# Kernel tuning notes

Hardware: AMD Instinct MI355X
Metric: run time of the kernel (lower is better)

Reference implementation:

```python
import jax, jax.numpy as jnp
import numpy as np
from jax.ops import segment_sum

N_NODES = 300000
N_EDGES = 600000
N_GRAPHS = 12000
HIDDEN = 128
F_ATOM, V_ATOM, D_ATOM = 9, 119, 9
F_BOND, V_BOND, D_BOND = 3, 6, 3


def setup_inputs() -> dict:
    key = jax.random.key(0)
    ks = jax.random.split(key, 12)
    x = jax.random.randint(ks[0], (N_NODES, F_ATOM), 0, 100, dtype=jnp.int64 if jax.config.jax_enable_x64 else jnp.int32)
    edge_index = jax.random.randint(ks[1], (2, N_EDGES), 0, N_NODES)
    edge_attr = jax.random.randint(ks[2], (N_EDGES, F_BOND), 0, 5)
    batch = jnp.sort(jax.random.randint(ks[3], (N_NODES,), 0, N_GRAPHS))
    s = 0.02
    atom_emb = jax.random.normal(ks[4], (F_ATOM, V_ATOM, D_ATOM), jnp.float32) * s
    bond_emb = jax.random.normal(ks[5], (F_BOND, V_BOND, D_BOND), jnp.float32) * s
    W1 = jax.random.normal(ks[6], (D_ATOM, HIDDEN), jnp.float32) * (1.0 / np.sqrt(D_ATOM))
    b1 = jnp.zeros((HIDDEN,), jnp.float32)
    W2 = jax.random.normal(ks[7], (HIDDEN, HIDDEN), jnp.float32) * (1.0 / np.sqrt(HIDDEN))
    b2 = jnp.zeros((HIDDEN,), jnp.float32)
    Wfc = jax.random.normal(ks[8], (HIDDEN, 128), jnp.float32) * (1.0 / np.sqrt(HIDDEN))
    bfc = jnp.zeros((128,), jnp.float32)
    return {"x": x, "edge_index": edge_index, "edge_attr": edge_attr, "batch": batch,
            "atom_emb": atom_emb, "bond_emb": bond_emb,
            "W1": W1, "b1": b1, "W2": W2, "b2": b2, "Wfc": Wfc, "bfc": bfc}


def _multi_embed(tables, idx):
    # tables: [F, V, D], idx: [N, F] -> sum over F of tables[f, idx[:, f]] -> [N, D]
    F = tables.shape[0]
    gathered = tables[jnp.arange(F)[None, :], idx]  # [N, F, D]
    return gathered.sum(axis=1)


def _gcn_conv(h, edge_index, W, b, n_nodes):
    # PyG GCNConv: add self-loops, symmetric deg^-1/2 normalization
    src, dst = edge_index[0], edge_index[1]
    deg = segment_sum(jnp.ones(src.shape[0], h.dtype), dst, num_segments=n_nodes) + 1.0  # self-loop
    dinv = jax.lax.rsqrt(deg)
    h = h @ W  # transform before propagation
    coef = (dinv[src] * dinv[dst])[:, None]
    agg = segment_sum(h[src] * coef, dst, num_segments=n_nodes)
    agg = agg + h * (dinv * dinv)[:, None]  # self-loop contribution (norm = 1/deg)
    return agg + b


def reference(x, edge_index, edge_attr, batch, atom_emb, bond_emb, W1, b1, W2, b2, Wfc, bfc):
    h = _multi_embed(atom_emb, x)            # AtomEncoder: [N, 9]
    _ = _multi_embed(bond_emb, edge_attr)    # BondEncoder (computed, unused downstream)
    h = _gcn_conv(h, edge_index, W1, b1, N_NODES)
    h = jax.nn.relu(h)
    h = _gcn_conv(h, edge_index, W2, b2, N_NODES)
    # global_mean_pool over graphs
    sums = segment_sum(h, batch, num_segments=N_GRAPHS)
    cnt = segment_sum(jnp.ones(N_NODES, h.dtype), batch, num_segments=N_GRAPHS)
    graph_emb = sums / jnp.clip(cnt, 1.0)[:, None]
    return graph_emb @ Wfc + bfc
```

## Files before the change

### kernel.cpp

```cpp
#include <hip/hip_runtime.h>

#define NN 300000
#define NE 600000
#define NG 12000
#define HH 128
#define FA 9
#define VA 119
#define DA 9
#define NCHUNK ((NN + 1023) / 1024)
#define POISON 0xAAAAAAAAu

#define HB  64
#define NCB 1172

#define OEMB 0
#define OW1  (FA*VA*DA)
#define OB1  (OW1 + DA*HH)
#define OW2  (OB1 + HH)
#define OB2  (OW2 + HH*HH)
#define OWFC (OB2 + HH)
#define OBFC (OWFC + HH*HH)
#define NWC  (OBFC + HH)

typedef unsigned short u16;
typedef unsigned int u32;
typedef __attribute__((ext_vector_type(8))) short bfrag8;
typedef __attribute__((ext_vector_type(16))) float ffrag16;

__device__ __forceinline__ float bf2f(u16 u){
  union { u32 i; float f; } v; v.i = ((u32)u) << 16; return v.f;
}
__device__ __forceinline__ float bflo(u32 w){
  union { u32 i; float f; } v; v.i = w << 16; return v.f;
}
__device__ __forceinline__ float bfhi(u32 w){
  union { u32 i; float f; } v; v.i = w & 0xFFFF0000u; return v.f;
}
__device__ __forceinline__ u16 f2bf(float f){
  union { float f; u32 i; } v; v.f = f;
  u32 x = v.i;
  return (u16)((x + 0x7FFFu + ((x >> 16) & 1u)) >> 16);
}
__device__ __forceinline__ float ldf(const void* p, int i, int isf32){
  return isf32 ? ((const float*)p)[i] : bf2f(((const u16*)p)[i]);
}
__device__ __forceinline__ int detect_isf32(const u16* emb16, int t, int* scnt){
  if (t == 0) *scnt = 0;
  __syncthreads();
  u16 u = emb16[t];
  int e = (u >> 7) & 0xFF;
  if (e >= 96 && e < 126) atomicAdd(scnt, 1);
  __syncthreads();
  return (*scnt >= 200) ? 0 : 1;
}

__global__ void k_pre(const int* __restrict__ x, const void* emb, const void* W1,
                      const void* b1, const void* W2, const void* b2,
                      const void* Wfc, const void* bfc,
                      const int* __restrict__ batch, const int* __restrict__ dst,
                      int* __restrict__ flag, float* __restrict__ wc,
                      u32* __restrict__ degcur, u16* __restrict__ rank,
                      int* __restrict__ gstart, uint4* __restrict__ h0a,
                      u32* __restrict__ h0b, float* __restrict__ wcomb,
                      float* __restrict__ bcomb, u32* __restrict__ btab2){
  __shared__ float embS[FA * VA * DA];
  __shared__ int scnt;
  int t = threadIdx.x;

  if (blockIdx.x < HB){
    int htid = blockIdx.x * 256 + t;
    const int4* d4 = (const int4*)dst;
    uint2* r2 = (uint2*)rank;
    #pragma unroll 2
    for (int i = htid; i < NE / 4; i += HB * 256){
      int4 v = d4[i];
      u32 r0 = atomicAdd(&degcur[v.x], 1u);
      u32 r1 = atomicAdd(&degcur[v.y], 1u);
      u32 rr2 = atomicAdd(&degcur[v.z], 1u);
      u32 rr3 = atomicAdd(&degcur[v.w], 1u);
      uint2 pk;
      pk.x = (u32)(u16)(r0 - POISON) | (((u32)(u16)(r1 - POISON)) << 16);
      pk.y = (u32)(u16)(rr2 - POISON) | (((u32)(u16)(rr3 - POISON)) << 16);
      r2[i] = pk;
    }
    return;
  }

  int isf32 = detect_isf32((const u16*)emb, t, &scnt);
  int tid = (blockIdx.x - HB) * 256 + t;
  int nth = NCB * 256;
  if (tid == 0) flag[0] = isf32;

  if (isf32){
    const float4* e4 = (const float4*)emb;
    for (int i = t; i < (FA*VA*DA)/4; i += 256){
      float4 v = e4[i];
      int o = i * 4;
      embS[o+0] = v.x; embS[o+1] = v.y; embS[o+2] = v.z; embS[o+3] = v.w;
    }
    if (t < 3) embS[9636 + t] = ((const float*)emb)[9636 + t];
  } else {
    const uint4* e4 = (const uint4*)emb;
    for (int i = t; i < (FA*VA*DA)/8; i += 256){
      uint4 v = e4[i];
      int o = i * 8;
      embS[o+0] = bflo(v.x); embS[o+1] = bfhi(v.x);
      embS[o+2] = bflo(v.y); embS[o+3] = bfhi(v.y);
      embS[o+4] = bflo(v.z); embS[o+5] = bfhi(v.z);
      embS[o+6] = bflo(v.w); embS[o+7] = bfhi(v.w);
    }
    if (t < 7) embS[9632 + t] = bf2f(((const u16*)emb)[9632 + t]);
  }

  for (int i = tid; i < NWC; i += nth){
    float v;
    if      (i < OW1)  v = ldf(emb, i - OEMB, isf32);
    else if (i < OB1)  v = ldf(W1,  i - OW1,  isf32);
    else if (i < OW2)  v = ldf(b1,  i - OB1,  isf32);
    else if (i < OB2)  v = ldf(W2,  i - OW2,  isf32);
    else if (i < OWFC) v = ldf(b2,  i - OB2,  isf32);
    else if (i < OBFC) v = ldf(Wfc, i - OWFC, isf32);
    else               v = ldf(bfc, i - OBFC, isf32);
    wc[i] = v;
  }

  if (tid < HH * HH){
    int d = tid >> 7, k = tid & 127;
    float s = 0.f;
    #pragma unroll 4
    for (int j = 0; j < HH; ++j) s += ldf(W2, d * HH + j, isf32) * ldf(Wfc, j * HH + k, isf32);
    wcomb[tid] = s;
    if (tid < HH){
      float sb = 0.f;
      #pragma unroll 4
      for (int j = 0; j < HH; ++j) sb += ldf(b2, j, isf32) * ldf(Wfc, j * HH + tid, isf32);
      bcomb[tid] = sb;
    }
    if (tid < 1024){
      int lane = tid >> 4, idx = tid & 15;
      int tile = idx >> 2, reg = idx & 3;
      int half = lane >> 5, col = lane & 31;
      int nn = tile * 32 + col;
      int k0 = half * 8 + reg * 2;
      int k1 = k0 + 1;
      u32 lo = 0, hi = 0;
      if (k0 < 9)       lo = f2bf(ldf(W1, k0 * HH + nn, isf32));
      else if (k0 == 9) lo = f2bf(ldf(b1, nn, isf32));
      if (k1 < 9)       hi = f2bf(ldf(W1, k1 * HH + nn, isf32));
      else if (k1 == 9) hi = f2bf(ldf(b1, nn, isf32));
      btab2[tid] = lo | (hi << 16);
    }
  }

  __syncthreads();
  int n = tid;
  if (n <= NG){
    if (n == NG) gstart[NG] = NN;
    else {
      int lo = 0, hi = NN;
      while (lo < hi){
        int mid = (lo + hi) >> 1;
        if (batch[mid] < n) lo = mid + 1; else hi = mid;
      }
      gstart[n] = lo;
    }
  }
  if (n >= NN) return;
  int idx[FA];
  #pragma unroll
  for (int f = 0; f < FA; ++f) idx[f] = x[n * FA + f];
  float acc[DA];
  #pragma unroll
  for (int d = 0; d < DA; ++d){
    float a = 0.f;
    #pragma unroll
    for (int f = 0; f < FA; ++f) a += embS[(f * VA + idx[f]) * DA + d];
    acc[d] = a;
  }
  uint4 pv;
  pv.x = (u32)f2bf(acc[0]) | ((u32)f2bf(acc[1]) << 16);
  pv.y = (u32)f2bf(acc[2]) | ((u32)f2bf(acc[3]) << 16);
  pv.z = (u32)f2bf(acc[4]) | ((u32)f2bf(acc[5]) << 16);
  pv.w = (u32)f2bf(acc[6]) | ((u32)f2bf(acc[7]) << 16);
  h0a[n] = pv;
  h0b[n] = (u32)f2bf(acc[8]);
}

__global__ void k_scan(const u32* __restrict__ degp, int* __restrict__ rowoff,
                       float* __restrict__ dinv, u32* __restrict__ sync){
  __shared__ int sh[256];
  __shared__ int sbase;
  int b = blockIdx.x;
  int t = threadIdx.x;
  int i0 = b * 1024 + t * 4;
  int v0=0, v1=0, v2=0, v3=0;
  if (i0 + 0 < NN){ v0 = (int)(degp[i0 + 0] - POISON); dinv[i0 + 0] = rsqrtf((float)v0 + 1.0f); }
  if (i0 + 1 < NN){ v1 = (int)(degp[i0 + 1] - POISON); dinv[i0 + 1] = rsqrtf((float)v1 + 1.0f); }
  if (i0 + 2 < NN){ v2 = (int)(degp[i0 + 2] - POISON); dinv[i0 + 2] = rsqrtf((float)v2 + 1.0f); }
  if (i0 + 3 < NN){ v3 = (int)(degp[i0 + 3] - POISON); dinv[i0 + 3] = rsqrtf((float)v3 + 1.0f); }
  int tsum = v0 + v1 + v2 + v3;
  sh[t] = tsum;
  __syncthreads();
  for (int off = 1; off < 256; off <<= 1){
    int add = (t >= off) ? sh[t - off] : 0;
    __syncthreads();
    sh[t] += add;
    __syncthreads();
  }
  int run = sh[t] - tsum;
  int tot = sh[255];

  if (t == 0){
    u32 w = (b == 0) ? ((3u << 30) | (u32)tot) : ((1u << 30) | (u32)tot);
    __hip_atomic_store(&sync[b], w, __ATOMIC_RELAXED, __HIP_MEMORY_SCOPE_AGENT);
    if (b == 0) sbase = 0;
  }
  if (b > 0 && t >= 192){
    int lane = t & 63;
    int running = 0;
    int p = b - 1;
    for (;;){
      int q = p - lane;
      u32 w = (q >= 0)
            ? __hip_atomic_load(&sync[q], __ATOMIC_RELAXED, __HIP_MEMORY_SCOPE_AGENT)
            : (3u << 30);
      u32 st = w >> 30;
      int val = (int)(w & 0x3FFFFFFFu);
      unsigned long long bi = __ballot(st == 3u);
      unsigned long long bg = __ballot(st == 1u);
      if (bi){
        int L = (int)(__ffsll((long long)bi) - 1);
        unsigned long long need = (L == 0) ? 0ull : ((1ull << L) - 1ull);
        if ((bg & need) == need){
          int contrib = (lane <= L) ? val : 0;
          #pragma unroll
          for (int off = 1; off < 64; off <<= 1) contrib += __shfl_xor(contrib, off, 64);
          running += contrib;
          break;
        }
      } else if (bg == ~0ull){
        int contrib = val;
        #pragma unroll
        for (int off = 1; off < 64; off <<= 1) contrib += __shfl_xor(contrib, off, 64);
        running += contrib;
        p -= 64;
      }
    }
    if (lane == 0){
      sbase = running;
      __hip_atomic_store(&sync[b], (3u << 30) | (u32)(running + tot),
                         __ATOMIC_RELAXED, __HIP_MEMORY_SCOPE_AGENT);
    }
  }
  __syncthreads();
  int gb = sbase;
  run += gb;
  if (i0 + 0 <= NN) rowoff[i0 + 0] = run;
  run += v0;
  if (i0 + 1 <= NN) rowoff[i0 + 1] = run;
  run += v1;
  if (i0 + 2 <= NN) rowoff[i0 + 2] = run;
  run += v2;
  if (i0 + 3 <= NN) rowoff[i0 + 3] = run;
}

__global__ void k_fill(const int* __restrict__ src, const int* __restrict__ dst,
                       const u16* __restrict__ rank, const int* __restrict__ rowoff,
                       const float* __restrict__ dinv, uint2* __restrict__ csr){
  int e = blockIdx.x * 256 + threadIdx.x;
  if (e < NE){
    int s = src[e], d = dst[e];
    int pos = rowoff[d] + (int)rank[e];
    uint2 ent;
    ent.x = (u32)s;
    ent.y = __float_as_uint(dinv[s] * dinv[d]);
    csr[pos] = ent;
  }
}

__global__ void k_l1csr(const uint4* __restrict__ h0a, const u32* __restrict__ h0b,
                        uint4* __restrict__ agg1a, u32* __restrict__ agg1b,
                        const int* __restrict__ rowoff,
                        const uint2* __restrict__ csr, const float* __restrict__ dinv){
  int n = blockIdx.x * 256 + threadIdx.x;
  if (n >= NN) return;
  float di = dinv[n];
  float c0 = di * di;
  float acc[DA];
  {
    uint4 ra = h0a[n];
    u32 r4 = h0b[n];
    acc[0]=c0*bflo(ra.x); acc[1]=c0*bfhi(ra.x); acc[2]=c0*bflo(ra.y); acc[3]=c0*bfhi(ra.y);
    acc[4]=c0*bflo(ra.z); acc[5]=c0*bfhi(ra.z); acc[6]=c0*bflo(ra.w); acc[7]=c0*bfhi(ra.w);
    acc[8]=c0*bflo(r4);
  }
  int s0 = rowoff[n], s1 = rowoff[n + 1];
  #pragma unroll 2
  for (int j = s0; j < s1; ++j){
    uint2 ent = csr[j];
    int s = (int)ent.x;
    float c = __uint_as_float(ent.y);
    uint4 ra = h0a[s];
    u32 r4 = h0b[s];
    acc[0]+=c*bflo(ra.x); acc[1]+=c*bfhi(ra.x); acc[2]+=c*bflo(ra.y); acc[3]+=c*bfhi(ra.y);
    acc[4]+=c*bflo(ra.z); acc[5]+=c*bfhi(ra.z); acc[6]+=c*bflo(ra.w); acc[7]+=c*bfhi(ra.w);
    acc[8]+=c*bflo(r4);
  }
  uint4 pv;
  pv.x = (u32)f2bf(acc[0]) | ((u32)f2bf(acc[1]) << 16);
  pv.y = (u32)f2bf(acc[2]) | ((u32)f2bf(acc[3]) << 16);
  pv.z = (u32)f2bf(acc[4]) | ((u32)f2bf(acc[5]) << 16);
  pv.w = (u32)f2bf(acc[6]) | ((u32)f2bf(acc[7]) << 16);
  agg1a[n] = pv;
  agg1b[n] = (u32)f2bf(acc[8]) | (0x3F80u << 16);
}

__global__ void k_l2pool(const uint4* __restrict__ agg1a, const u32* __restrict__ agg1b,
                         const float* __restrict__ dinv,
                         const int* __restrict__ rowoff,
                         const uint2* __restrict__ csr, const int* __restrict__ gstart,
                         const u32* __restrict__ btab2, float* __restrict__ pooled){
  int t = threadIdx.x;
  int g = blockIdx.x * 4 + (t >> 6);
  int lane = t & 63;
  if (g >= NG) return;
  u32 bf[16];
  {
    const u32* bp = btab2 + lane * 16;
    #pragma unroll
    for (int i = 0; i < 16; ++i) bf[i] = bp[i];
  }
  int a = gstart[g], b = gstart[g + 1];
  int j0 = rowoff[a], j1 = rowoff[b];
  int nself = b - a;
  int M = nself + (j1 - j0);
  float s[4] = {0.f, 0.f, 0.f, 0.f};
  int half = lane >> 5;
  int li = lane & 31;

  for (int base = 0; base < M; base += 32){
    int i = base + li;
    u32 a0 = 0, a1 = 0, a2 = 0, a3 = 0;
    float coef = 0.f;
    if (i < M){
      int n;
      if (i < nself){
        n = a + i;
        float dn = dinv[n];
        coef = dn * dn;
      } else {
        uint2 e = csr[j0 + (i - nself)];
        n = (int)e.x;
        coef = __uint_as_float(e.y);
      }
      if (half == 0){
        uint4 ra = agg1a[n];
        a0 = ra.x; a1 = ra.y; a2 = ra.z; a3 = ra.w;
      } else {
        a0 = agg1b[n];
      }
    }
    float cf[16];
    #pragma unroll
    for (int reg = 0; reg < 16; ++reg){
      int row = (reg & 3) + 8 * (reg >> 2) + 4 * half;
      cf[reg] = __shfl(coef, row, 64);
    }
    union { u32 u[4]; bfrag8 v; } au;
    au.u[0] = a0; au.u[1] = a1; au.u[2] = a2; au.u[3] = a3;
    #pragma unroll
    for (int tile = 0; tile < 4; ++tile){
      union { u32 u[4]; bfrag8 v; } bu;
      bu.u[0] = bf[tile*4+0]; bu.u[1] = bf[tile*4+1];
      bu.u[2] = bf[tile*4+2]; bu.u[3] = bf[tile*4+3];
      ffrag16 c;
      #pragma unroll
      for (int q = 0; q < 16; ++q) c[q] = 0.f;
      c = __builtin_amdgcn_mfma_f32_32x32x16_bf16(au.v, bu.v, c, 0, 0, 0);
      float acc = 0.f;
      #pragma unroll
      for (int reg = 0; reg < 16; ++reg)
        acc += fmaxf(c[reg], 0.f) * cf[reg];
      s[tile] += acc;
    }
  }
  #pragma unroll
  for (int tile = 0; tile < 4; ++tile){
    float v = s[tile];
    v += __shfl_xor(v, 32, 64);
    s[tile] = v;
  }
  if (half == 0){
    #pragma unroll
    for (int tile = 0; tile < 4; ++tile)
      pooled[(size_t)g * HH + tile * 32 + li] = s[tile];
  }
}

__global__ void k_head(const float* __restrict__ pooled, const float* __restrict__ wcomb,
                       const float* __restrict__ bcomb, const float* __restrict__ wc,
                       const int* __restrict__ gstart, const int* __restrict__ flag,
                       void* __restrict__ out){
  __shared__ float wS[HH * HH];
  __shared__ float pl[2][HH];
  int t = threadIdx.x;
  for (int i = t; i < HH * HH; i += 256) wS[i] = wcomb[i];
  __syncthreads();
  int isf32 = flag[0];
  int gg = t >> 7, k = t & 127;
  for (int p = blockIdx.x; p < NG / 2; p += gridDim.x){
    int g = p * 2 + gg;
    int cnt = gstart[g + 1] - gstart[g];
    float inv = 1.0f / (float)(cnt > 1 ? cnt : 1);
    pl[gg][k] = pooled[(size_t)g * HH + k] * inv;
    __syncthreads();
    float acc = wc[OBFC + k] + (cnt > 0 ? bcomb[k] : 0.f);
    #pragma unroll 8
    for (int d = 0; d < HH; ++d) acc += pl[gg][d] * wS[d * HH + k];
    if (isf32) ((float*)out)[(size_t)g * HH + k] = acc;
    else       ((u16*)out)[(size_t)g * HH + k] = f2bf(acc);
    __syncthreads();
  }
}

extern "C" void kernel_launch(void* const* d_in, const int* in_sizes, int n_in,
                              void* d_out, int out_size, void* d_ws, size_t ws_size,
                              hipStream_t stream){
  const int* x     = (const int*)d_in[0];
  const int* ei    = (const int*)d_in[1];
  const int* batch = (const int*)d_in[3];
  const void* aemb = d_in[4];
  const void* W1   = d_in[6];
  const void* b1   = d_in[7];
  const void* W2   = d_in[8];
  const void* b2   = d_in[9];
  const void* Wfc  = d_in[10];
  const void* bfc  = d_in[11];
  const int* srcp = ei;
  const int* dstp = ei + NE;

  char* p = (char*)d_ws;
  int*   flag   = (int*)p;                 p += 64;
  float* wc     = (float*)p;               p += sizeof(float) * 43944;
  float* wcomb  = (float*)p;               p += sizeof(float) * (HH * HH);
  float* bcomb  = (float*)p;               p += sizeof(float) * HH;
  u32*   btab2  = (u32*)p;                 p += sizeof(u32) * 1024;
  u32*   degcur = (u32*)p;                 p += sizeof(u32) * (NN + 16);
  int*   rowoff = (int*)p;                 p += sizeof(int) * (NN + 4);
  u32*   sync   = (u32*)p;                 p += sizeof(u32) * 512;
  float* dinv   = (float*)p;               p += sizeof(float) * NN;
  u16*   rank   = (u16*)p;                 p += sizeof(u16) * (NE + 8);
  uint2* csr    = (uint2*)p;               p += sizeof(uint2) * NE;
  int*   gstart = (int*)p;                 p += sizeof(int) * (NG + 4);
  float* pooled = (float*)p;               p += sizeof(float) * (size_t)NG * HH;
  uint4* h0a    = (uint4*)p;               p += sizeof(uint4) * NN;
  u32*   h0b    = (u32*)p;                 p += sizeof(u32) * NN;
  uint4* agg1a  = (uint4*)p;               p += sizeof(uint4) * NN;
  u32*   agg1b  = (u32*)p;                 p += sizeof(u32) * NN;
  (void)p; (void)ws_size; (void)n_in; (void)in_sizes; (void)out_size;

  k_pre   <<<HB + NCB, 256, 0, stream>>>(x, aemb, W1, b1, W2, b2, Wfc, bfc,
                                         batch, dstp, flag, wc, degcur, rank,
                                         gstart, h0a, h0b, wcomb, bcomb, btab2);
  k_scan  <<<NCHUNK, 256, 0, stream>>>(degcur, rowoff, dinv, sync);
  k_fill  <<<(NE + 255) / 256, 256, 0, stream>>>(srcp, dstp, rank, rowoff, dinv, csr);
  k_l1csr <<<(NN + 255) / 256, 256, 0, stream>>>(h0a, h0b, agg1a, agg1b, rowoff, csr, dinv);
  k_l2pool<<<NG / 4, 256, 0, stream>>>(agg1a, agg1b, dinv, rowoff, csr, gstart,
                                       btab2, pooled);
  k_head  <<<512, 256, 0, stream>>>(pooled, wcomb, bcomb, wc, gstart, flag, d_out);
}
```

Before: 217.5 us.

## Pack node features into 32-byte records and software-pipeline layer-2 gathers

Node embeddings and layer-1 aggregates now live in one interleaved 32-byte record per node instead of split 16-byte and 4-byte arrays. The self-loop coefficient dinv^2 is stored inside that record, so layer 2 no longer gathers dinv separately. The layer-2 pooling kernel prefetches the edge entries and feature rows two waves ahead to hide gather latency, and layer 1 unrolls its edge loop by two explicitly. k_pre gets more histogram blocks and fewer embedding blocks, with a grid-stride loop over nodes. The records double the footprint of the split arrays and carry padding bytes.

```diff
diff --git a/kernel.cpp b/kernel.cpp
--- a/kernel.cpp
+++ b/kernel.cpp
@@ -10,8 +10,9 @@
 #define NCHUNK ((NN + 1023) / 1024)
 #define POISON 0xAAAAAAAAu
 
-#define HB  64
-#define NCB 1172
+#define HB  128
+#define NCB 896
+#define NTH (NCB * 256)
 
 #define OEMB 0
 #define OW1  (FA*VA*DA)
@@ -60,8 +61,8 @@
                       const int* __restrict__ batch, const int* __restrict__ dst,
                       int* __restrict__ flag, float* __restrict__ wc,
                       u32* __restrict__ degcur, u16* __restrict__ rank,
-                      int* __restrict__ gstart, uint4* __restrict__ h0a,
-                      u32* __restrict__ h0b, float* __restrict__ wcomb,
+                      int* __restrict__ gstart, uint4* __restrict__ h0p,
+                      float* __restrict__ wcomb,
                       float* __restrict__ bcomb, u32* __restrict__ btab2){
   __shared__ float embS[FA * VA * DA];
   __shared__ int scnt;
@@ -88,7 +89,6 @@
 
   int isf32 = detect_isf32((const u16*)emb, t, &scnt);
   int tid = (blockIdx.x - HB) * 256 + t;
-  int nth = NCB * 256;
   if (tid == 0) flag[0] = isf32;
 
   if (isf32){
@@ -112,7 +112,7 @@
     if (t < 7) embS[9632 + t] = bf2f(((const u16*)emb)[9632 + t]);
   }
 
-  for (int i = tid; i < NWC; i += nth){
+  for (int i = tid; i < NWC; i += NTH){
     float v;
     if      (i < OW1)  v = ldf(emb, i - OEMB, isf32);
     else if (i < OB1)  v = ldf(W1,  i - OW1,  isf32);
@@ -153,8 +153,8 @@
   }
 
   __syncthreads();
-  int n = tid;
-  if (n <= NG){
+  if (tid <= NG){
+    int n = tid;
     if (n == NG) gstart[NG] = NN;
     else {
       int lo = 0, hi = NN;
@@ -165,25 +165,26 @@
       gstart[n] = lo;
     }
   }
-  if (n >= NN) return;
-  int idx[FA];
-  #pragma unroll
-  for (int f = 0; f < FA; ++f) idx[f] = x[n * FA + f];
-  float acc[DA];
-  #pragma unroll
-  for (int d = 0; d < DA; ++d){
-    float a = 0.f;
-    #pragma unroll
-    for (int f = 0; f < FA; ++f) a += embS[(f * VA + idx[f]) * DA + d];
-    acc[d] = a;
-  }
-  uint4 pv;
-  pv.x = (u32)f2bf(acc[0]) | ((u32)f2bf(acc[1]) << 16);
-  pv.y = (u32)f2bf(acc[2]) | ((u32)f2bf(acc[3]) << 16);
-  pv.z = (u32)f2bf(acc[4]) | ((u32)f2bf(acc[5]) << 16);
-  pv.w = (u32)f2bf(acc[6]) | ((u32)f2bf(acc[7]) << 16);
-  h0a[n] = pv;
-  h0b[n] = (u32)f2bf(acc[8]);
+  for (int n = tid; n < NN; n += NTH){
+    int idx[FA];
+    #pragma unroll
+    for (int f = 0; f < FA; ++f) idx[f] = x[n * FA + f];
+    float acc[DA];
+    #pragma unroll
+    for (int d = 0; d < DA; ++d){
+      float a = 0.f;
+      #pragma unroll
+      for (int f = 0; f < FA; ++f) a += embS[(f * VA + idx[f]) * DA + d];
+      acc[d] = a;
+    }
+    uint4 pv;
+    pv.x = (u32)f2bf(acc[0]) | ((u32)f2bf(acc[1]) << 16);
+    pv.y = (u32)f2bf(acc[2]) | ((u32)f2bf(acc[3]) << 16);
+    pv.z = (u32)f2bf(acc[4]) | ((u32)f2bf(acc[5]) << 16);
+    pv.w = (u32)f2bf(acc[6]) | ((u32)f2bf(acc[7]) << 16);
+    h0p[2 * n] = pv;
+    h0p[2 * n + 1] = make_uint4((u32)f2bf(acc[8]), 0u, 0u, 0u);
+  }
 }
 
 __global__ void k_scan(const u32* __restrict__ degp, int* __restrict__ rowoff,
@@ -278,45 +279,62 @@
   }
 }
 
-__global__ void k_l1csr(const uint4* __restrict__ h0a, const u32* __restrict__ h0b,
-                        uint4* __restrict__ agg1a, u32* __restrict__ agg1b,
+__global__ void k_l1csr(const uint4* __restrict__ h0p, uint4* __restrict__ agg1p,
                         const int* __restrict__ rowoff,
                         const uint2* __restrict__ csr, const float* __restrict__ dinv){
   int n = blockIdx.x * 256 + threadIdx.x;
   if (n >= NN) return;
   float di = dinv[n];
   float c0 = di * di;
+  const u32* h0w = (const u32*)h0p;
   float acc[DA];
   {
-    uint4 ra = h0a[n];
-    u32 r4 = h0b[n];
+    uint4 ra = h0p[2 * n];
+    u32 r4 = h0w[8 * n + 4];
     acc[0]=c0*bflo(ra.x); acc[1]=c0*bfhi(ra.x); acc[2]=c0*bflo(ra.y); acc[3]=c0*bfhi(ra.y);
     acc[4]=c0*bflo(ra.z); acc[5]=c0*bfhi(ra.z); acc[6]=c0*bflo(ra.w); acc[7]=c0*bfhi(ra.w);
     acc[8]=c0*bflo(r4);
   }
   int s0 = rowoff[n], s1 = rowoff[n + 1];
-  #pragma unroll 2
-  for (int j = s0; j < s1; ++j){
-    uint2 ent = csr[j];
-    int s = (int)ent.x;
-    float c = __uint_as_float(ent.y);
-    uint4 ra = h0a[s];
-    u32 r4 = h0b[s];
-    acc[0]+=c*bflo(ra.x); acc[1]+=c*bfhi(ra.x); acc[2]+=c*bflo(ra.y); acc[3]+=c*bfhi(ra.y);
-    acc[4]+=c*bflo(ra.z); acc[5]+=c*bfhi(ra.z); acc[6]+=c*bflo(ra.w); acc[7]+=c*bfhi(ra.w);
-    acc[8]+=c*bflo(r4);
+  int j = s0;
+  for (; j + 2 <= s1; j += 2){
+    uint2 e0 = csr[j], e1 = csr[j + 1];
+    int sA = (int)e0.x, sB = (int)e1.x;
+    float cA = __uint_as_float(e0.y), cB = __uint_as_float(e1.y);
+    uint4 ra = h0p[2 * sA];
+    u32 r4 = h0w[8 * sA + 4];
+    uint4 rb = h0p[2 * sB];
+    u32 q4 = h0w[8 * sB + 4];
+    acc[0]+=cA*bflo(ra.x); acc[1]+=cA*bfhi(ra.x); acc[2]+=cA*bflo(ra.y); acc[3]+=cA*bfhi(ra.y);
+    acc[4]+=cA*bflo(ra.z); acc[5]+=cA*bfhi(ra.z); acc[6]+=cA*bflo(ra.w); acc[7]+=cA*bfhi(ra.w);
+    acc[8]+=cA*bflo(r4);
+    acc[0]+=cB*bflo(rb.x); acc[1]+=cB*bfhi(rb.x); acc[2]+=cB*bflo(rb.y); acc[3]+=cB*bfhi(rb.y);
+    acc[4]+=cB*bflo(rb.z); acc[5]+=cB*bfhi(rb.z); acc[6]+=cB*bflo(rb.w); acc[7]+=cB*bfhi(rb.w);
+    acc[8]+=cB*bflo(q4);
+  }
+  if (j < s1){
+    uint2 e0 = csr[j];
+    int sA = (int)e0.x;
+    float cA = __uint_as_float(e0.y);
+    uint4 ra = h0p[2 * sA];
+    u32 r4 = h0w[8 * sA + 4];
+    acc[0]+=cA*bflo(ra.x); acc[1]+=cA*bfhi(ra.x); acc[2]+=cA*bflo(ra.y); acc[3]+=cA*bfhi(ra.y);
+    acc[4]+=cA*bflo(ra.z); acc[5]+=cA*bfhi(ra.z); acc[6]+=cA*bflo(ra.w); acc[7]+=cA*bfhi(ra.w);
+    acc[8]+=cA*bflo(r4);
   }
   uint4 pv;
   pv.x = (u32)f2bf(acc[0]) | ((u32)f2bf(acc[1]) << 16);
   pv.y = (u32)f2bf(acc[2]) | ((u32)f2bf(acc[3]) << 16);
   pv.z = (u32)f2bf(acc[4]) | ((u32)f2bf(acc[5]) << 16);
   pv.w = (u32)f2bf(acc[6]) | ((u32)f2bf(acc[7]) << 16);
-  agg1a[n] = pv;
-  agg1b[n] = (u32)f2bf(acc[8]) | (0x3F80u << 16);
-}
-
-__global__ void k_l2pool(const uint4* __restrict__ agg1a, const u32* __restrict__ agg1b,
-                         const float* __restrict__ dinv,
+  agg1p[2 * n] = pv;
+  agg1p[2 * n + 1] = make_uint4((u32)f2bf(acc[8]) | (0x3F80u << 16),
+                                __float_as_uint(c0), 0u, 0u);
+}
+
+struct EIt { int n; float ec; int self; };
+
+__global__ void k_l2pool(const uint4* __restrict__ agg1p,
                          const int* __restrict__ rowoff,
                          const uint2* __restrict__ csr, const int* __restrict__ gstart,
                          const u32* __restrict__ btab2, float* __restrict__ pooled){
@@ -338,33 +356,45 @@
   int half = lane >> 5;
   int li = lane & 31;
 
-  for (int base = 0; base < M; base += 32){
-    int i = base + li;
-    u32 a0 = 0, a1 = 0, a2 = 0, a3 = 0;
-    float coef = 0.f;
-    if (i < M){
-      int n;
-      if (i < nself){
-        n = a + i;
-        float dn = dinv[n];
-        coef = dn * dn;
-      } else {
-        uint2 e = csr[j0 + (i - nself)];
-        n = (int)e.x;
-        coef = __uint_as_float(e.y);
-      }
-      if (half == 0){
-        uint4 ra = agg1a[n];
-        a0 = ra.x; a1 = ra.y; a2 = ra.z; a3 = ra.w;
-      } else {
-        a0 = agg1b[n];
-      }
+  auto loadE = [&](int i) -> EIt {
+    EIt e; e.self = (i < nself) ? 1 : 0; e.ec = 0.f;
+    if (e.self) e.n = a + i;
+    else if (i < M){
+      uint2 tt = csr[j0 + (i - nself)];
+      e.n = (int)tt.x; e.ec = __uint_as_float(tt.y);
+    } else e.n = a;
+    return e;
+  };
+
+  int W = (M + 31) >> 5;
+  EIt e0, e1, e2; uint4 A0, A1;
+  e0.n = a; e0.ec = 0.f; e0.self = 0; e1 = e0; e2 = e0;
+  A0 = make_uint4(0,0,0,0); A1 = A0;
+  if (W > 0){
+    e0 = loadE(li);
+    A0 = agg1p[2 * e0.n + half];
+    if (W > 1) e1 = loadE(32 + li);
+  }
+  for (int w = 0; w < W; ++w){
+    if (w + 1 < W) A1 = agg1p[2 * e1.n + half];
+    if (w + 2 < W) e2 = loadE((w + 2) * 32 + li);
+
+    int i = w * 32 + li;
+    u32 a0, a1, a2, a3;
+    float coef;
+    if (half == 0){
+      int v = (i < M) ? 1 : 0;
+      a0 = v ? A0.x : 0u; a1 = v ? A0.y : 0u; a2 = v ? A0.z : 0u; a3 = v ? A0.w : 0u;
+      coef = 0.f;
+    } else {
+      a0 = (i < M) ? A0.x : 0u; a1 = a2 = a3 = 0u;
+      coef = e0.self ? __uint_as_float(A0.y) : e0.ec;
     }
     float cf[16];
     #pragma unroll
     for (int reg = 0; reg < 16; ++reg){
       int row = (reg & 3) + 8 * (reg >> 2) + 4 * half;
-      cf[reg] = __shfl(coef, row, 64);
+      cf[reg] = __shfl(coef, row + 32, 64);
     }
     union { u32 u[4]; bfrag8 v; } au;
     au.u[0] = a0; au.u[1] = a1; au.u[2] = a2; au.u[3] = a3;
@@ -383,6 +413,7 @@
         acc += fmaxf(c[reg], 0.f) * cf[reg];
       s[tile] += acc;
     }
+    e0 = e1; A0 = A1; e1 = e2;
   }
   #pragma unroll
   for (int tile = 0; tile < 4; ++tile){
@@ -453,19 +484,16 @@
   uint2* csr    = (uint2*)p;               p += sizeof(uint2) * NE;
   int*   gstart = (int*)p;                 p += sizeof(int) * (NG + 4);
   float* pooled = (float*)p;               p += sizeof(float) * (size_t)NG * HH;
-  uint4* h0a    = (uint4*)p;               p += sizeof(uint4) * NN;
-  u32*   h0b    = (u32*)p;                 p += sizeof(u32) * NN;
-  uint4* agg1a  = (uint4*)p;               p += sizeof(uint4) * NN;
-  u32*   agg1b  = (u32*)p;                 p += sizeof(u32) * NN;
+  uint4* h0p    = (uint4*)p;               p += sizeof(uint4) * 2 * NN;
+  uint4* agg1p  = (uint4*)p;               p += sizeof(uint4) * 2 * NN;
   (void)p; (void)ws_size; (void)n_in; (void)in_sizes; (void)out_size;
 
   k_pre   <<<HB + NCB, 256, 0, stream>>>(x, aemb, W1, b1, W2, b2, Wfc, bfc,
                                          batch, dstp, flag, wc, degcur, rank,
-                                         gstart, h0a, h0b, wcomb, bcomb, btab2);
+                                         gstart, h0p, wcomb, bcomb, btab2);
   k_scan  <<<NCHUNK, 256, 0, stream>>>(degcur, rowoff, dinv, sync);
   k_fill  <<<(NE + 255) / 256, 256, 0, stream>>>(srcp, dstp, rank, rowoff, dinv, csr);
-  k_l1csr <<<(NN + 255) / 256, 256, 0, stream>>>(h0a, h0b, agg1a, agg1b, rowoff, csr, dinv);
-  k_l2pool<<<NG / 4, 256, 0, stream>>>(agg1a, agg1b, dinv, rowoff, csr, gstart,
-                                       btab2, pooled);
+  k_l1csr <<<(NN + 255) / 256, 256, 0, stream>>>(h0p, agg1p, rowoff, csr, dinv);
+  k_l2pool<<<NG / 4, 256, 0, stream>>>(agg1p, rowoff, csr, gstart, btab2, pooled);
   k_head  <<<512, 256, 0, stream>>>(pooled, wcomb, bcomb, wc, gstart, flag, d_out);
 }
```

After: 230.1 us. 1.06x slower.

## Privatize degree counters per XCD with workgroup-scope atomics

Applied to the files above, without the earlier changes.

The degree-counting atomics now go to a private counter slice per XCD, chosen from the hardware XCC id register, and use workgroup-scope atomics so they can resolve in that XCD's local L2 instead of a device-coherent point. The scan kernel merges the eight slices into the total degree and stores a per-node, per-XCD base offset. The fill kernel combines that base with a 13-bit local rank to place each CSR entry. The preprocessing grid is also rebalanced to more histogram blocks, with a grid-stride embedding loop, and the counter slices share workspace with later buffers. The cost is extra scan traffic from reading eight slices, an extra gather in the fill kernel, and a reliance on the workspace being re-poisoned and on workgroup-scope atomics behaving correctly across blocks.

```diff
diff --git a/kernel.cpp b/kernel.cpp
--- a/kernel.cpp
+++ b/kernel.cpp
@@ -10,8 +10,9 @@
 #define NCHUNK ((NN + 1023) / 1024)
 #define POISON 0xAAAAAAAAu
 
-#define HB  64
-#define NCB 1172
+#define HB  128
+#define NCB 896
+#define NTH (NCB * 256)
 
 #define OEMB 0
 #define OW1  (FA*VA*DA)
@@ -22,6 +23,8 @@
 #define OBFC (OWFC + HH*HH)
 #define NWC  (OBFC + HH)
 
+#define XCCID_IMM ((3 << 11) | (0 << 6) | 20)
+
 typedef unsigned short u16;
 typedef unsigned int u32;
 typedef __attribute__((ext_vector_type(8))) short bfrag8;
@@ -59,7 +62,7 @@
                       const void* Wfc, const void* bfc,
                       const int* __restrict__ batch, const int* __restrict__ dst,
                       int* __restrict__ flag, float* __restrict__ wc,
-                      u32* __restrict__ degcur, u16* __restrict__ rank,
+                      u32* __restrict__ degcur8, u16* __restrict__ rank,
                       int* __restrict__ gstart, uint4* __restrict__ h0a,
                       u32* __restrict__ h0b, float* __restrict__ wcomb,
                       float* __restrict__ bcomb, u32* __restrict__ btab2){
@@ -68,19 +71,22 @@
   int t = threadIdx.x;
 
   if (blockIdx.x < HB){
+    int xcd = (int)(__builtin_amdgcn_s_getreg(XCCID_IMM)) & 7;
+    u32* slice = degcur8 + (size_t)xcd * NN;
+    u32 xh = (u32)xcd << 13;
     int htid = blockIdx.x * 256 + t;
     const int4* d4 = (const int4*)dst;
     uint2* r2 = (uint2*)rank;
     #pragma unroll 2
     for (int i = htid; i < NE / 4; i += HB * 256){
       int4 v = d4[i];
-      u32 r0 = atomicAdd(&degcur[v.x], 1u);
-      u32 r1 = atomicAdd(&degcur[v.y], 1u);
-      u32 rr2 = atomicAdd(&degcur[v.z], 1u);
-      u32 rr3 = atomicAdd(&degcur[v.w], 1u);
+      u32 r0 = __hip_atomic_fetch_add(&slice[v.x], 1u, __ATOMIC_RELAXED, __HIP_MEMORY_SCOPE_WORKGROUP);
+      u32 r1 = __hip_atomic_fetch_add(&slice[v.y], 1u, __ATOMIC_RELAXED, __HIP_MEMORY_SCOPE_WORKGROUP);
+      u32 rA = __hip_atomic_fetch_add(&slice[v.z], 1u, __ATOMIC_RELAXED, __HIP_MEMORY_SCOPE_WORKGROUP);
+      u32 rB = __hip_atomic_fetch_add(&slice[v.w], 1u, __ATOMIC_RELAXED, __HIP_MEMORY_SCOPE_WORKGROUP);
       uint2 pk;
-      pk.x = (u32)(u16)(r0 - POISON) | (((u32)(u16)(r1 - POISON)) << 16);
-      pk.y = (u32)(u16)(rr2 - POISON) | (((u32)(u16)(rr3 - POISON)) << 16);
+      pk.x = (((r0 - POISON) & 0x1FFFu) | xh) | (((((r1 - POISON) & 0x1FFFu) | xh)) << 16);
+      pk.y = (((rA - POISON) & 0x1FFFu) | xh) | (((((rB - POISON) & 0x1FFFu) | xh)) << 16);
       r2[i] = pk;
     }
     return;
@@ -88,7 +94,6 @@
 
   int isf32 = detect_isf32((const u16*)emb, t, &scnt);
   int tid = (blockIdx.x - HB) * 256 + t;
-  int nth = NCB * 256;
   if (tid == 0) flag[0] = isf32;
 
   if (isf32){
@@ -112,7 +117,7 @@
     if (t < 7) embS[9632 + t] = bf2f(((const u16*)emb)[9632 + t]);
   }
 
-  for (int i = tid; i < NWC; i += nth){
+  for (int i = tid; i < NWC; i += NTH){
     float v;
     if      (i < OW1)  v = ldf(emb, i - OEMB, isf32);
     else if (i < OB1)  v = ldf(W1,  i - OW1,  isf32);
@@ -153,8 +158,8 @@
   }
 
   __syncthreads();
-  int n = tid;
-  if (n <= NG){
+  if (tid <= NG){
+    int n = tid;
     if (n == NG) gstart[NG] = NN;
     else {
       int lo = 0, hi = NN;
@@ -165,39 +170,68 @@
       gstart[n] = lo;
     }
   }
-  if (n >= NN) return;
-  int idx[FA];
-  #pragma unroll
-  for (int f = 0; f < FA; ++f) idx[f] = x[n * FA + f];
-  float acc[DA];
-  #pragma unroll
-  for (int d = 0; d < DA; ++d){
-    float a = 0.f;
-    #pragma unroll
-    for (int f = 0; f < FA; ++f) a += embS[(f * VA + idx[f]) * DA + d];
-    acc[d] = a;
-  }
-  uint4 pv;
-  pv.x = (u32)f2bf(acc[0]) | ((u32)f2bf(acc[1]) << 16);
-  pv.y = (u32)f2bf(acc[2]) | ((u32)f2bf(acc[3]) << 16);
-  pv.z = (u32)f2bf(acc[4]) | ((u32)f2bf(acc[5]) << 16);
-  pv.w = (u32)f2bf(acc[6]) | ((u32)f2bf(acc[7]) << 16);
-  h0a[n] = pv;
-  h0b[n] = (u32)f2bf(acc[8]);
+  for (int n = tid; n < NN; n += NTH){
+    int idx[FA];
+    #pragma unroll
+    for (int f = 0; f < FA; ++f) idx[f] = x[n * FA + f];
+    float acc[DA];
+    #pragma unroll
+    for (int d = 0; d < DA; ++d){
+      float a = 0.f;
+      #pragma unroll
+      for (int f = 0; f < FA; ++f) a += embS[(f * VA + idx[f]) * DA + d];
+      acc[d] = a;
+    }
+    uint4 pv;
+    pv.x = (u32)f2bf(acc[0]) | ((u32)f2bf(acc[1]) << 16);
+    pv.y = (u32)f2bf(acc[2]) | ((u32)f2bf(acc[3]) << 16);
+    pv.z = (u32)f2bf(acc[4]) | ((u32)f2bf(acc[5]) << 16);
+    pv.w = (u32)f2bf(acc[6]) | ((u32)f2bf(acc[7]) << 16);
+    h0a[n] = pv;
+    h0b[n] = (u32)f2bf(acc[8]);
+  }
 }
 
 __global__ void k_scan(const u32* __restrict__ degp, int* __restrict__ rowoff,
-                       float* __restrict__ dinv, u32* __restrict__ sync){
+                       float* __restrict__ dinv, u32* __restrict__ sync,
+                       u16* __restrict__ xcdbase){
   __shared__ int sh[256];
   __shared__ int sbase;
   int b = blockIdx.x;
   int t = threadIdx.x;
   int i0 = b * 1024 + t * 4;
   int v0=0, v1=0, v2=0, v3=0;
-  if (i0 + 0 < NN){ v0 = (int)(degp[i0 + 0] - POISON); dinv[i0 + 0] = rsqrtf((float)v0 + 1.0f); }
-  if (i0 + 1 < NN){ v1 = (int)(degp[i0 + 1] - POISON); dinv[i0 + 1] = rsqrtf((float)v1 + 1.0f); }
-  if (i0 + 2 < NN){ v2 = (int)(degp[i0 + 2] - POISON); dinv[i0 + 2] = rsqrtf((float)v2 + 1.0f); }
-  if (i0 + 3 < NN){ v3 = (int)(degp[i0 + 3] - POISON); dinv[i0 + 3] = rsqrtf((float)v3 + 1.0f); }
+  if (i0 < NN){
+    u32 cc[8][4];
+    const uint4* d4 = (const uint4*)degp;
+    #pragma unroll
+    for (int xx = 0; xx < 8; ++xx){
+      uint4 w = d4[((size_t)xx * NN + (size_t)i0) >> 2];
+      cc[xx][0] = w.x - POISON; cc[xx][1] = w.y - POISON;
+      cc[xx][2] = w.z - POISON; cc[xx][3] = w.w - POISON;
+    }
+    int vv[4];
+    #pragma unroll
+    for (int k = 0; k < 4; ++k){
+      vv[k] = 0;
+      int n = i0 + k;
+      if (n < NN){
+        int run = 0;
+        u16 b8[8];
+        #pragma unroll
+        for (int xx = 0; xx < 8; ++xx){ b8[xx] = (u16)run; run += (int)cc[xx][k]; }
+        vv[k] = run;
+        dinv[n] = rsqrtf((float)run + 1.0f);
+        uint4 pk;
+        pk.x = (u32)b8[0] | ((u32)b8[1] << 16);
+        pk.y = (u32)b8[2] | ((u32)b8[3] << 16);
+        pk.z = (u32)b8[4] | ((u32)b8[5] << 16);
+        pk.w = (u32)b8[6] | ((u32)b8[7] << 16);
+        ((uint4*)xcdbase)[n] = pk;
+      }
+    }
+    v0 = vv[0]; v1 = vv[1]; v2 = vv[2]; v3 = vv[3];
+  }
   int tsum = v0 + v1 + v2 + v3;
   sh[t] = tsum;
   __syncthreads();
@@ -266,11 +300,13 @@
 
 __global__ void k_fill(const int* __restrict__ src, const int* __restrict__ dst,
                        const u16* __restrict__ rank, const int* __restrict__ rowoff,
+                       const u16* __restrict__ xcdbase,
                        const float* __restrict__ dinv, uint2* __restrict__ csr){
   int e = blockIdx.x * 256 + threadIdx.x;
   if (e < NE){
     int s = src[e], d = dst[e];
-    int pos = rowoff[d] + (int)rank[e];
+    u32 rk = rank[e];
+    int pos = rowoff[d] + (int)xcdbase[((size_t)d << 3) | (rk >> 13)] + (int)(rk & 0x1FFFu);
     uint2 ent;
     ent.x = (u32)s;
     ent.y = __float_as_uint(dinv[s] * dinv[d]);
@@ -445,25 +481,28 @@
   float* wcomb  = (float*)p;               p += sizeof(float) * (HH * HH);
   float* bcomb  = (float*)p;               p += sizeof(float) * HH;
   u32*   btab2  = (u32*)p;                 p += sizeof(u32) * 1024;
-  u32*   degcur = (u32*)p;                 p += sizeof(u32) * (NN + 16);
+  char*  unionA = p;
+  uint4* agg1a  = (uint4*)unionA;
+  u32*   agg1b  = (u32*)(unionA + sizeof(uint4) * NN);
+  float* pooled = (float*)(unionA + sizeof(uint4) * NN + sizeof(u32) * NN);
+  u32*   degcur8= (u32*)unionA;
+  p += sizeof(uint4) * NN + sizeof(u32) * NN + sizeof(float) * (size_t)NG * HH;
   int*   rowoff = (int*)p;                 p += sizeof(int) * (NN + 4);
   u32*   sync   = (u32*)p;                 p += sizeof(u32) * 512;
   float* dinv   = (float*)p;               p += sizeof(float) * NN;
   u16*   rank   = (u16*)p;                 p += sizeof(u16) * (NE + 8);
   uint2* csr    = (uint2*)p;               p += sizeof(uint2) * NE;
   int*   gstart = (int*)p;                 p += sizeof(int) * (NG + 4);
-  float* pooled = (float*)p;               p += sizeof(float) * (size_t)NG * HH;
+  u16*   xcdbase= (u16*)p;                 p += sizeof(u16) * (size_t)8 * NN;
   uint4* h0a    = (uint4*)p;               p += sizeof(uint4) * NN;
   u32*   h0b    = (u32*)p;                 p += sizeof(u32) * NN;
-  uint4* agg1a  = (uint4*)p;               p += sizeof(uint4) * NN;
-  u32*   agg1b  = (u32*)p;                 p += sizeof(u32) * NN;
   (void)p; (void)ws_size; (void)n_in; (void)in_sizes; (void)out_size;
 
   k_pre   <<<HB + NCB, 256, 0, stream>>>(x, aemb, W1, b1, W2, b2, Wfc, bfc,
-                                         batch, dstp, flag, wc, degcur, rank,
+                                         batch, dstp, flag, wc, degcur8, rank,
                                          gstart, h0a, h0b, wcomb, bcomb, btab2);
-  k_scan  <<<NCHUNK, 256, 0, stream>>>(degcur, rowoff, dinv, sync);
-  k_fill  <<<(NE + 255) / 256, 256, 0, stream>>>(srcp, dstp, rank, rowoff, dinv, csr);
+  k_scan  <<<NCHUNK, 256, 0, stream>>>(degcur8, rowoff, dinv, sync, xcdbase);
+  k_fill  <<<(NE + 255) / 256, 256, 0, stream>>>(srcp, dstp, rank, rowoff, xcdbase, dinv, csr);
   k_l1csr <<<(NN + 255) / 256, 256, 0, stream>>>(h0a, h0b, agg1a, agg1b, rowoff, csr, dinv);
   k_l2pool<<<NG / 4, 256, 0, stream>>>(agg1a, agg1b, dinv, rowoff, csr, gstart,
                                        btab2, pooled);
```

After: 233.7 us. 7.5% more time.
